# Kernel tuning notes

Hardware: AMD Instinct MI355X
Metric: run time of the kernel (lower is better)

## Reference

```python
import jax, jax.numpy as jnp
import numpy as np

H2 = 1.0  # self.bandwidth = bandwidth**2 with bandwidth=1.0

Q, N, D = 4096, 65536, 32


def setup_inputs() -> dict:
    key = jax.random.key(0)
    k1, k2, k3 = jax.random.split(key, 3)
    X = jax.random.normal(k1, (Q, D), dtype=jnp.float32)
    X_train = jax.random.normal(k2, (N, D), dtype=jnp.float32)
    sample_weight = jax.random.uniform(k3, (N,), dtype=jnp.float32)  # non-negative
    return {"X": X, "X_train": X_train, "sample_weight": sample_weight}


def reference(X, X_train, sample_weight):
    # Brute-force ('standard'/RootTree) KDE: every query sees all train points.
    d = X.shape[-1]
    d2 = (jnp.sum(X * X, axis=-1, keepdims=True)
          + jnp.sum(X_train * X_train, axis=-1)[None, :]
          - 2.0 * (X @ X_train.T))
    # GaussianKernel(diff) = (2*pi)^{-d/2} exp(-||diff||^2 / (2*H2))
    log_k = -0.5 * d2 / H2 - 0.5 * d * jnp.log(jnp.float32(2.0 * np.pi))
    # log( sum_j w_j K_ij / (bw_norm * sum_j w_j) ), bw_norm = H2**(d/2)
    log_num = jax.scipy.special.logsumexp(log_k + jnp.log(sample_weight)[None, :], axis=-1)
    log_norm = 0.5 * d * jnp.log(jnp.float32(H2)) + jnp.log(jnp.sum(sample_weight))
    return log_num - log_norm
```

## Files before the change

kernel.cpp:

```cpp
#include <hip/hip_runtime.h>

#define QN 4096
#define NN 65536
#define DD 32

typedef __attribute__((ext_vector_type(8))) _Float16 half8;
typedef __attribute__((ext_vector_type(4))) _Float16 half4v;
typedef __attribute__((ext_vector_type(4))) float floatx4;

#define LOG2E 1.4426950408889634f
#define HALF_D_LOG_2PI 29.40603306254953f


__global__ __launch_bounds__(256) void prep_all(
    const float* __restrict__ X, const float* __restrict__ Xt,
    const float* __restrict__ w, _Float16* __restrict__ Xh,
    float* __restrict__ qn, _Float16* __restrict__ Xth,
    float* __restrict__ c, float* __restrict__ sumw) {
    const int b = blockIdx.x;
    if (b < 128) {
        int tid  = b * 256 + threadIdx.x;
        int row  = tid >> 3;
        int part = tid & 7;
        const float4 v = ((const float4*)X)[row * 8 + part];
        float nrm = v.x * v.x + v.y * v.y + v.z * v.z + v.w * v.w;
        nrm += __shfl_xor(nrm, 1);
        nrm += __shfl_xor(nrm, 2);
        nrm += __shfl_xor(nrm, 4);
        half4v h = { (_Float16)(v.x * LOG2E), (_Float16)(v.y * LOG2E),
                     (_Float16)(v.z * LOG2E), (_Float16)(v.w * LOG2E) };
        *(half4v*)(Xh + row * DD + part * 4) = h;
        if (part == 0) qn[row] = 0.5f * nrm;
    } else if (b < 2176) {
        int tid  = (b - 128) * 256 + threadIdx.x;
        int row  = tid >> 3;
        int part = tid & 7;
        const float4 v = ((const float4*)Xt)[row * 8 + part];
        float nrm = v.x * v.x + v.y * v.y + v.z * v.z + v.w * v.w;
        nrm += __shfl_xor(nrm, 1);
        nrm += __shfl_xor(nrm, 2);
        nrm += __shfl_xor(nrm, 4);
        half4v h = { (_Float16)v.x, (_Float16)v.y, (_Float16)v.z, (_Float16)v.w };
        *(half4v*)(Xth + row * DD + part * 4) = h;
        if (part == 0)
            c[row] = w[row] * __builtin_amdgcn_exp2f(-0.5f * LOG2E * nrm);
    } else {
        int bid = b - 2176;
        float v = 0.f;
        for (int i = bid * 256 + threadIdx.x; i < NN; i += 64 * 256)
            v += w[i];
        #pragma unroll
        for (int o = 1; o < 64; o <<= 1) v += __shfl_xor(v, o);
        __shared__ float red[4];
        if ((threadIdx.x & 63) == 0) red[threadIdx.x >> 6] = v;
        __syncthreads();
        if (threadIdx.x == 0) atomicAdd(sumw, red[0] + red[1] + red[2] + red[3]);
    }
}

__global__ __launch_bounds__(256) void kde_main(
    const _Float16* __restrict__ Xh, const _Float16* __restrict__ Xth,
    const float* __restrict__ c, float* __restrict__ S) {
    const int lane   = threadIdx.x & 63;
    const int wave   = threadIdx.x >> 6;
    const int quad   = lane >> 4;
    const int l16    = lane & 15;
    const int m_base = blockIdx.x * 256 + wave * 64;
    const int n_beg  = blockIdx.y * 512;

    half8 a[4];
    #pragma unroll
    for (int t = 0; t < 4; ++t)
        a[t] = *(const half8*)(Xh + (m_base + t * 16 + l16) * DD + quad * 8);

    float s[4][4] = {};
    const floatx4 zero = {0.f, 0.f, 0.f, 0.f};

    const _Float16* bp = Xth + (size_t)(n_beg + l16) * DD + quad * 8;
    const float*    cp = c + n_beg + l16;

    for (int it = 0; it < 32; ++it) {
        half8 bfrag = *(const half8*)bp;
        float cv    = *cp;
        #pragma unroll
        for (int t = 0; t < 4; ++t) {
            floatx4 g = __builtin_amdgcn_mfma_f32_16x16x32_f16(a[t], bfrag, zero, 0, 0, 0);
            #pragma unroll
            for (int r = 0; r < 4; ++r)
                s[t][r] += cv * __builtin_amdgcn_exp2f(g[r]);
        }
        bp += 16 * DD;
        cp += 16;
    }

    #pragma unroll
    for (int t = 0; t < 4; ++t) {
        #pragma unroll
        for (int r = 0; r < 4; ++r) {
            float v = s[t][r];
            v += __shfl_xor(v, 1);
            v += __shfl_xor(v, 2);
            v += __shfl_xor(v, 4);
            v += __shfl_xor(v, 8);
            if (l16 == 0)
                atomicAdd(&S[m_base + t * 16 + quad * 4 + r], v);
        }
    }
}

__global__ void finalize(const float* __restrict__ S, const float* __restrict__ qn,
                         const float* __restrict__ sumw, float* __restrict__ out) {
    int i = blockIdx.x * blockDim.x + threadIdx.x;
    out[i] = logf(S[i]) - qn[i] - HALF_D_LOG_2PI - logf(*sumw);
}

extern "C" void kernel_launch(void* const* d_in, const int* in_sizes, int n_in,
                              void* d_out, int out_size, void* d_ws, size_t ws_size,
                              hipStream_t stream) {
    const float* X  = (const float*)d_in[0];
    const float* Xt = (const float*)d_in[1];
    const float* w  = (const float*)d_in[2];
    float* out = (float*)d_out;

    char* ws = (char*)d_ws;
    _Float16* Xh   = (_Float16*)(ws);
    _Float16* Xth  = (_Float16*)(ws + 262144);
    float*    c    = (float*)(ws + 4456448);
    float*    qn   = (float*)(ws + 4718592);
    float*    S    = (float*)(ws + 4734976);
    float*    sumw = (float*)(ws + 4751360);

    hipMemsetAsync(S, 0, QN * sizeof(float) + sizeof(float), stream);

    prep_all<<<2240, 256, 0, stream>>>(X, Xt, w, Xh, qn, Xth, c, sumw);
    kde_main<<<dim3(QN / 256, 128), 256, 0, stream>>>(Xh, Xth, c, S);
    finalize<<<QN / 256, 256, 0, stream>>>(S, qn, sumw, out);
}
```

Before: 116.0 us.

## Fuse finalize into main kernel, drop memset, enlarge per-wave query tile

Zeroes the accumulator and completion counter inside the prep kernel instead of a memset. The finalize step moves into kde_main via a last-block-done atomic counter, and the weight-sum atomic becomes per-block partials. Each wave now covers 128 queries over a 256-column strip, and the next B fragment is prefetched. This removes launch overhead and raises operand reuse, at the cost of more registers and a serial tail in the last block.

```diff
diff --git a/kernel.cpp b/kernel.cpp
--- a/kernel.cpp
+++ b/kernel.cpp
@@ -1,8 +1,15 @@
 #include <hip/hip_runtime.h>
+#include <math.h>
 
 #define QN 4096
 #define NN 65536
 #define DD 32
+
+#define GRID_X 8
+#define GRID_Y 256
+#define STRIP  256
+#define ITERS  16
+#define NBLK   (GRID_X * GRID_Y)
 
 typedef __attribute__((ext_vector_type(8))) _Float16 half8;
 typedef __attribute__((ext_vector_type(4))) _Float16 half4v;
@@ -16,7 +23,8 @@
     const float* __restrict__ X, const float* __restrict__ Xt,
     const float* __restrict__ w, _Float16* __restrict__ Xh,
     float* __restrict__ qn, _Float16* __restrict__ Xth,
-    float* __restrict__ c, float* __restrict__ sumw) {
+    float* __restrict__ c, float* __restrict__ S,
+    float* __restrict__ swp, unsigned* __restrict__ done) {
     const int b = blockIdx.x;
     if (b < 128) {
         int tid  = b * 256 + threadIdx.x;
@@ -31,6 +39,8 @@
                      (_Float16)(v.z * LOG2E), (_Float16)(v.w * LOG2E) };
         *(half4v*)(Xh + row * DD + part * 4) = h;
         if (part == 0) qn[row] = 0.5f * nrm;
+        if (tid < QN) S[tid] = 0.f;
+        if (tid == QN) *done = 0u;
     } else if (b < 2176) {
         int tid  = (b - 128) * 256 + threadIdx.x;
         int row  = tid >> 3;
@@ -54,47 +64,53 @@
         __shared__ float red[4];
         if ((threadIdx.x & 63) == 0) red[threadIdx.x >> 6] = v;
         __syncthreads();
-        if (threadIdx.x == 0) atomicAdd(sumw, red[0] + red[1] + red[2] + red[3]);
+        if (threadIdx.x == 0) swp[bid] = red[0] + red[1] + red[2] + red[3];
     }
 }
 
 __global__ __launch_bounds__(256) void kde_main(
     const _Float16* __restrict__ Xh, const _Float16* __restrict__ Xth,
-    const float* __restrict__ c, float* __restrict__ S) {
+    const float* __restrict__ c, float* __restrict__ S,
+    const float* __restrict__ qn, const float* __restrict__ swp,
+    unsigned* __restrict__ done, float* __restrict__ out) {
     const int lane   = threadIdx.x & 63;
     const int wave   = threadIdx.x >> 6;
     const int quad   = lane >> 4;
     const int l16    = lane & 15;
-    const int m_base = blockIdx.x * 256 + wave * 64;
-    const int n_beg  = blockIdx.y * 512;
+    const int m_base = blockIdx.x * 512 + wave * 128;
+    const int n_beg  = blockIdx.y * STRIP;
 
-    half8 a[4];
+    half8 a[8];
     #pragma unroll
-    for (int t = 0; t < 4; ++t)
+    for (int t = 0; t < 8; ++t)
         a[t] = *(const half8*)(Xh + (m_base + t * 16 + l16) * DD + quad * 8);
 
-    float s[4][4] = {};
+    float s[8][4] = {};
     const floatx4 zero = {0.f, 0.f, 0.f, 0.f};
 
     const _Float16* bp = Xth + (size_t)(n_beg + l16) * DD + quad * 8;
     const float*    cp = c + n_beg + l16;
+    half8 bcur = *(const half8*)bp;
+    float ccur = *cp;
 
-    for (int it = 0; it < 32; ++it) {
-        half8 bfrag = *(const half8*)bp;
-        float cv    = *cp;
+    for (int it = 0; it < ITERS; ++it) {
+        bp += 16 * DD;
+        cp += 16;
+        half8 bnext = *(const half8*)bp;
+        float cnext = *cp;
         #pragma unroll
-        for (int t = 0; t < 4; ++t) {
-            floatx4 g = __builtin_amdgcn_mfma_f32_16x16x32_f16(a[t], bfrag, zero, 0, 0, 0);
+        for (int t = 0; t < 8; ++t) {
+            floatx4 g = __builtin_amdgcn_mfma_f32_16x16x32_f16(a[t], bcur, zero, 0, 0, 0);
             #pragma unroll
             for (int r = 0; r < 4; ++r)
-                s[t][r] += cv * __builtin_amdgcn_exp2f(g[r]);
+                s[t][r] += ccur * __builtin_amdgcn_exp2f(g[r]);
         }
-        bp += 16 * DD;
-        cp += 16;
+        bcur = bnext;
+        ccur = cnext;
     }
 
     #pragma unroll
-    for (int t = 0; t < 4; ++t) {
+    for (int t = 0; t < 8; ++t) {
         #pragma unroll
         for (int r = 0; r < 4; ++r) {
             float v = s[t][r];
@@ -106,12 +122,26 @@
                 atomicAdd(&S[m_base + t * 16 + quad * 4 + r], v);
         }
     }
-}
 
-__global__ void finalize(const float* __restrict__ S, const float* __restrict__ qn,
-                         const float* __restrict__ sumw, float* __restrict__ out) {
-    int i = blockIdx.x * blockDim.x + threadIdx.x;
-    out[i] = logf(S[i]) - qn[i] - HALF_D_LOG_2PI - logf(*sumw);
+    __threadfence();
+    __shared__ int last;
+    if (threadIdx.x == 0) {
+        unsigned cnt = atomicAdd(done, 1u);
+        last = (cnt == NBLK - 1) ? 1 : 0;
+    }
+    __syncthreads();
+    if (last) {
+        __threadfence();
+        float sw = 0.f;
+        #pragma unroll
+        for (int k = 0; k < 64; ++k) sw += swp[k];
+        float lsw = logf(sw);
+        for (int i = threadIdx.x; i < QN; i += 256) {
+            float Sv = __hip_atomic_load(&S[i], __ATOMIC_RELAXED,
+                                         __HIP_MEMORY_SCOPE_AGENT);
+            out[i] = logf(Sv) - qn[i] - HALF_D_LOG_2PI - lsw;
+        }
+    }
 }
 
 extern "C" void kernel_launch(void* const* d_in, const int* in_sizes, int n_in,
@@ -128,11 +158,10 @@
     float*    c    = (float*)(ws + 4456448);
     float*    qn   = (float*)(ws + 4718592);
     float*    S    = (float*)(ws + 4734976);
-    float*    sumw = (float*)(ws + 4751360);
+    float*    swp  = (float*)(ws + 4751360);
+    unsigned* done = (unsigned*)(ws + 4751616);
 
-    hipMemsetAsync(S, 0, QN * sizeof(float) + sizeof(float), stream);
-
-    prep_all<<<2240, 256, 0, stream>>>(X, Xt, w, Xh, qn, Xth, c, sumw);
-    kde_main<<<dim3(QN / 256, 128), 256, 0, stream>>>(Xh, Xth, c, S);
-    finalize<<<QN / 256, 256, 0, stream>>>(S, qn, sumw, out);
+    prep_all<<<2240, 256, 0, stream>>>(X, Xt, w, Xh, qn, Xth, c, S, swp, done);
+    kde_main<<<dim3(GRID_X, GRID_Y), 256, 0, stream>>>(Xh, Xth, c, S, qn, swp,
+                                                       done, out);
 }
```

Result: slower. 245.9 us (+111.9%).
